# Optimization experiments

Hardware: AMD Instinct MI355X
Metric: run time of the kernel (lower is better)

The kernel has to match this reference:

```python
import jax, jax.numpy as jnp
import numpy as np
from jax import lax

ALPHA = 1.0
NEG = -1.0e6  # sentinel 'no foreground' position; squared dist ~1e12 fits fp32


def _edt(fg):
    """Exact Euclidean distance transform: distance from every pixel to the
    nearest True pixel of fg [B, H, W] (0 where fg is True). Matches
    scipy.ndimage.distance_transform_edt(1 - mask) with mask = fg.
    Separable algorithm: exact 1D pass along W, then exact min over rows."""
    B, H, W = fg.shape
    xi = jnp.arange(W, dtype=jnp.float32)
    # nearest foreground to the LEFT (j <= i): max index j with fg
    pos_l = jnp.where(fg, xi, NEG)
    dl = xi - lax.cummax(pos_l, axis=2)
    # nearest foreground to the RIGHT (j >= i): min index j with fg
    pos_r = jnp.where(fg, -xi, NEG)
    right = lax.cummax(pos_r[..., ::-1], axis=2)[..., ::-1]  # = -min_{j>=i} j
    dr = -right - xi
    g2 = jnp.square(jnp.minimum(dl, dr))  # [B, H, W] squared 1D distance

    y = jnp.arange(H, dtype=jnp.float32)
    sq = jnp.square(y[:, None] - y[None, :])  # [H, H] (y - y')^2

    def col_pass(g2_img):  # [H, W] -> [H, W]
        # dt2[y, x] = min_{y'} g2[y', x] + (y - y')^2  (exact 2D EDT^2)
        return jnp.min(g2_img[None, :, :] + sq[:, :, None], axis=1)

    dt2 = lax.map(col_pass, g2)  # sequential over batch to bound memory
    return jnp.sqrt(dt2)


def setup_inputs() -> dict:
    key = jax.random.key(0)
    k1, k2 = jax.random.split(key)
    pred = jax.random.normal(k1, (16, 2, 256, 256), dtype=jnp.float32)
    target = jax.random.randint(k2, (16, 256, 256), 0, 2, dtype=jnp.int32)
    return {"pred": pred, "target": target}


def reference(pred, target):
    # pred: [B, C, H, W] logits; target: [B, H, W] binary int mask
    pred_lbl = jnp.argmax(pred, axis=1)  # [B, H, W] in {0, 1} (C == 2)
    pred_dt = lax.stop_gradient(_edt(pred_lbl == 1))
    tgt_dt = lax.stop_gradient(_edt(target == 1))
    hd_p2t = jnp.mean(pred_lbl.astype(jnp.float32) * tgt_dt)
    hd_t2p = jnp.mean(target.astype(jnp.float32) * pred_dt)
    return ALPHA * (hd_p2t + hd_t2p) / 2.0
```

## Files before the change

kernel.cpp:

```cpp
#include <hip/hip_runtime.h>
#include <hip/hip_bf16.h>
#include <math.h>


#define B 16
#define H 256
#define W 256
#define IMG (H * W)
#define NPIX (B * IMG)
#define NEGF (-1.0e6f)
#define NINF (-3.0e38f)
#define NBLK 2048

__global__ __launch_bounds__(256) void rowpass_kernel(
    const float* __restrict__ pred, const int* __restrict__ target,
    float* __restrict__ g2, unsigned char* __restrict__ lbl) {
  const int lane = threadIdx.x & 63;
  const int wid = threadIdx.x >> 6;
  const int row = blockIdx.x * 4 + wid;
  const int m = row >> 12;
  const int bh = row & 4095;
  const int b = bh >> 8;
  const int y = bh & 255;
  const int x0 = lane * 4;

  bool fg[4];
  if (m == 0) {
    const float* base = pred + (size_t)b * (2 * IMG) + y * W + x0;
    const float4 c0 = *(const float4*)(base);
    const float4 c1 = *(const float4*)(base + IMG);
    fg[0] = c1.x > c0.x; fg[1] = c1.y > c0.y;
    fg[2] = c1.z > c0.z; fg[3] = c1.w > c0.w;
  } else {
    const int4 tv = *(const int4*)(target + (size_t)b * IMG + y * W + x0);
    fg[0] = tv.x == 1; fg[1] = tv.y == 1; fg[2] = tv.z == 1; fg[3] = tv.w == 1;
  }

  uchar4 lb;
  lb.x = fg[0]; lb.y = fg[1]; lb.z = fg[2]; lb.w = fg[3];
  *(uchar4*)(lbl + (size_t)m * NPIX + (size_t)b * IMG + y * W + x0) = lb;

  const float xf0 = (float)x0;

  float p0 = fg[0] ? xf0 : NEGF;
  float p1 = fmaxf(p0, fg[1] ? xf0 + 1.f : NEGF);
  float p2 = fmaxf(p1, fg[2] ? xf0 + 2.f : NEGF);
  float p3 = fmaxf(p2, fg[3] ? xf0 + 3.f : NEGF);
  float s = p3;
#pragma unroll
  for (int off = 1; off < 64; off <<= 1) {
    float u = __shfl_up(s, (unsigned)off);
    if (lane >= off) s = fmaxf(s, u);
  }
  float e = __shfl_up(s, 1u);
  if (lane == 0) e = NINF;
  const float dl0 = xf0 - fmaxf(e, p0);
  const float dl1 = xf0 + 1.f - fmaxf(e, p1);
  const float dl2 = xf0 + 2.f - fmaxf(e, p2);
  const float dl3 = xf0 + 3.f - fmaxf(e, p3);

  float q3 = fg[3] ? -(xf0 + 3.f) : NEGF;
  float q2 = fmaxf(q3, fg[2] ? -(xf0 + 2.f) : NEGF);
  float q1 = fmaxf(q2, fg[1] ? -(xf0 + 1.f) : NEGF);
  float q0 = fmaxf(q1, fg[0] ? -xf0 : NEGF);
  float t = q0;
#pragma unroll
  for (int off = 1; off < 64; off <<= 1) {
    float u = __shfl_down(t, (unsigned)off);
    if (lane < 64 - off) t = fmaxf(t, u);
  }
  float f = __shfl_down(t, 1u);
  if (lane == 63) f = NINF;
  const float dr0 = -fmaxf(f, q0) - xf0;
  const float dr1 = -fmaxf(f, q1) - (xf0 + 1.f);
  const float dr2 = -fmaxf(f, q2) - (xf0 + 2.f);
  const float dr3 = -fmaxf(f, q3) - (xf0 + 3.f);

  float4 o;
  float v;
  v = fminf(dl0, dr0); o.x = v * v;
  v = fminf(dl1, dr1); o.y = v * v;
  v = fminf(dl2, dr2); o.z = v * v;
  v = fminf(dl3, dr3); o.w = v * v;
  *(float4*)(g2 + (size_t)m * NPIX + (size_t)b * IMG + y * W + x0) = o;
}

__global__ __launch_bounds__(256) void colpass_kernel(
    const float* __restrict__ g2, const unsigned char* __restrict__ lbl,
    float* __restrict__ partials) {
  const int tid = threadIdx.x;
  const int bi = blockIdx.x;
  const int xt = bi & 3;
  const int yt = (bi >> 2) & 15;
  const int m = (bi >> 6) & 1;
  const int b = bi >> 7;
  const int xin = tid & 63;
  const int ysub = tid >> 6;
  const int x = xt * 64 + xin;
  const int y0 = yt * 16 + ysub * 4;

  const float* __restrict__ gimg = g2 + (size_t)m * NPIX + (size_t)b * IMG;

  float a0 = gimg[(y0 + 0) * W + x];
  float a1 = gimg[(y0 + 1) * W + x];
  float a2 = gimg[(y0 + 2) * W + x];
  float a3 = gimg[(y0 + 3) * W + x];

  const float U = fmaxf(fmaxf(a0, a1), fmaxf(a2, a3));
  const int r = (int)sqrtf(U) + 1;
  int lo = y0 - r; if (lo < 0) lo = 0;
  int hi = y0 + 3 + r; if (hi > H - 1) hi = H - 1;

  for (int yp = lo; yp <= hi; ++yp) {
    const float v = gimg[yp * W + x];
    const float d0 = (float)(y0 - yp);
    const float d1 = d0 + 1.f;
    const float d2 = d0 + 2.f;
    const float d3 = d0 + 3.f;
    a0 = fminf(a0, fmaf(d0, d0, v));
    a1 = fminf(a1, fmaf(d1, d1, v));
    a2 = fminf(a2, fmaf(d2, d2, v));
    a3 = fminf(a3, fmaf(d3, d3, v));
  }

  const unsigned char* wl =
      lbl + (size_t)(1 - m) * NPIX + (size_t)b * IMG + y0 * W + x;
  float local = 0.f;
  local += (float)wl[0 * W] * sqrtf(a0);
  local += (float)wl[1 * W] * sqrtf(a1);
  local += (float)wl[2 * W] * sqrtf(a2);
  local += (float)wl[3 * W] * sqrtf(a3);

  __shared__ float red[256];
  red[tid] = local;
  __syncthreads();
  for (int s = 128; s > 0; s >>= 1) {
    if (tid < s) red[tid] += red[tid + s];
    __syncthreads();
  }
  if (tid == 0) partials[bi] = red[0];
}

__global__ __launch_bounds__(256) void finalize_kernel(
    const float* __restrict__ partials, float* __restrict__ out) {
  const int tid = threadIdx.x;
  float s = 0.f;
#pragma unroll
  for (int i = 0; i < NBLK / 256; ++i) s += partials[i * 256 + tid];
  __shared__ float red[256];
  red[tid] = s;
  __syncthreads();
  for (int k = 128; k > 0; k >>= 1) {
    if (tid < k) red[tid] += red[tid + k];
    __syncthreads();
  }
  if (tid == 0) out[0] = red[0] * (0.5f / (float)NPIX);
}

extern "C" void kernel_launch(void* const* d_in, const int* in_sizes, int n_in,
                              void* d_out, int out_size, void* d_ws, size_t ws_size,
                              hipStream_t stream) {
  const float* pred = (const float*)d_in[0];
  const int* target = (const int*)d_in[1];
  float* out = (float*)d_out;

  float* g2 = (float*)d_ws;
  float* partials = g2 + 2 * (size_t)NPIX;
  unsigned char* lbl = (unsigned char*)(partials + NBLK);

  rowpass_kernel<<<2 * B * H / 4, 256, 0, stream>>>(pred, target, g2, lbl);
  colpass_kernel<<<NBLK, 256, 0, stream>>>(g2, lbl, partials);
  finalize_kernel<<<1, 256, 0, stream>>>(partials, out);
}
```

Measured before the change: 77.70 us.

## Fuse row pass, column pass and final reduction into one cooperative kernel

Merges the three launches into a single cooperative-launch kernel of 1024 persistent blocks, with grid-wide syncs between the row pass, the column pass and the final reduction. Each block now handles two row groups and two column tiles. This removes two kernel launch gaps and the separate finalize launch. In exchange it adds two grid barriers, which are costly across all CUs, and fixes the grid size, which must fit co-resident at 4 blocks per CU.

```diff
diff --git a/kernel.cpp b/kernel.cpp
--- a/kernel.cpp
+++ b/kernel.cpp
@@ -1,6 +1,9 @@
 #include <hip/hip_runtime.h>
 #include <hip/hip_bf16.h>
+#include <hip/hip_cooperative_groups.h>
 #include <math.h>
+
+namespace cg = cooperative_groups;
 
 
 #define B 16
@@ -10,151 +13,156 @@
 #define NPIX (B * IMG)
 #define NEGF (-1.0e6f)
 #define NINF (-3.0e38f)
-#define NBLK 2048
+#define GRID 1024
 
-__global__ __launch_bounds__(256) void rowpass_kernel(
+__global__ __launch_bounds__(256, 4) void fused_kernel(
     const float* __restrict__ pred, const int* __restrict__ target,
-    float* __restrict__ g2, unsigned char* __restrict__ lbl) {
-  const int lane = threadIdx.x & 63;
-  const int wid = threadIdx.x >> 6;
-  const int row = blockIdx.x * 4 + wid;
-  const int m = row >> 12;
-  const int bh = row & 4095;
-  const int b = bh >> 8;
-  const int y = bh & 255;
-  const int x0 = lane * 4;
+    float* __restrict__ g2, unsigned char* __restrict__ lbl,
+    float* __restrict__ partials, float* __restrict__ out) {
+  cg::grid_group grid = cg::this_grid();
+  const int tid = threadIdx.x;
+  const int lane = tid & 63;
+  const int wid = tid >> 6;
+  __shared__ float red[256];
 
-  bool fg[4];
-  if (m == 0) {
-    const float* base = pred + (size_t)b * (2 * IMG) + y * W + x0;
-    const float4 c0 = *(const float4*)(base);
-    const float4 c1 = *(const float4*)(base + IMG);
-    fg[0] = c1.x > c0.x; fg[1] = c1.y > c0.y;
-    fg[2] = c1.z > c0.z; fg[3] = c1.w > c0.w;
-  } else {
-    const int4 tv = *(const int4*)(target + (size_t)b * IMG + y * W + x0);
-    fg[0] = tv.x == 1; fg[1] = tv.y == 1; fg[2] = tv.z == 1; fg[3] = tv.w == 1;
+#pragma unroll
+  for (int i = 0; i < 2; ++i) {
+    const int row = blockIdx.x * 8 + i * 4 + wid;
+    const int m = row >> 12;
+    const int bh = row & 4095;
+    const int b = bh >> 8;
+    const int y = bh & 255;
+    const int x0 = lane * 4;
+
+    bool fg[4];
+    if (m == 0) {
+      const float* base = pred + (size_t)b * (2 * IMG) + y * W + x0;
+      const float4 c0 = *(const float4*)(base);
+      const float4 c1 = *(const float4*)(base + IMG);
+      fg[0] = c1.x > c0.x; fg[1] = c1.y > c0.y;
+      fg[2] = c1.z > c0.z; fg[3] = c1.w > c0.w;
+    } else {
+      const int4 tv = *(const int4*)(target + (size_t)b * IMG + y * W + x0);
+      fg[0] = tv.x == 1; fg[1] = tv.y == 1; fg[2] = tv.z == 1; fg[3] = tv.w == 1;
+    }
+
+    uchar4 lb;
+    lb.x = fg[0]; lb.y = fg[1]; lb.z = fg[2]; lb.w = fg[3];
+    *(uchar4*)(lbl + (size_t)m * NPIX + (size_t)b * IMG + y * W + x0) = lb;
+
+    const float xf0 = (float)x0;
+
+    float p0 = fg[0] ? xf0 : NEGF;
+    float p1 = fmaxf(p0, fg[1] ? xf0 + 1.f : NEGF);
+    float p2 = fmaxf(p1, fg[2] ? xf0 + 2.f : NEGF);
+    float p3 = fmaxf(p2, fg[3] ? xf0 + 3.f : NEGF);
+    float s = p3;
+#pragma unroll
+    for (int off = 1; off < 64; off <<= 1) {
+      float u = __shfl_up(s, (unsigned)off);
+      if (lane >= off) s = fmaxf(s, u);
+    }
+    float e = __shfl_up(s, 1u);
+    if (lane == 0) e = NINF;
+    const float dl0 = xf0 - fmaxf(e, p0);
+    const float dl1 = xf0 + 1.f - fmaxf(e, p1);
+    const float dl2 = xf0 + 2.f - fmaxf(e, p2);
+    const float dl3 = xf0 + 3.f - fmaxf(e, p3);
+
+    float q3 = fg[3] ? -(xf0 + 3.f) : NEGF;
+    float q2 = fmaxf(q3, fg[2] ? -(xf0 + 2.f) : NEGF);
+    float q1 = fmaxf(q2, fg[1] ? -(xf0 + 1.f) : NEGF);
+    float q0 = fmaxf(q1, fg[0] ? -xf0 : NEGF);
+    float t = q0;
+#pragma unroll
+    for (int off = 1; off < 64; off <<= 1) {
+      float u = __shfl_down(t, (unsigned)off);
+      if (lane < 64 - off) t = fmaxf(t, u);
+    }
+    float f = __shfl_down(t, 1u);
+    if (lane == 63) f = NINF;
+    const float dr0 = -fmaxf(f, q0) - xf0;
+    const float dr1 = -fmaxf(f, q1) - (xf0 + 1.f);
+    const float dr2 = -fmaxf(f, q2) - (xf0 + 2.f);
+    const float dr3 = -fmaxf(f, q3) - (xf0 + 3.f);
+
+    float4 o;
+    float v;
+    v = fminf(dl0, dr0); o.x = v * v;
+    v = fminf(dl1, dr1); o.y = v * v;
+    v = fminf(dl2, dr2); o.z = v * v;
+    v = fminf(dl3, dr3); o.w = v * v;
+    *(float4*)(g2 + (size_t)m * NPIX + (size_t)b * IMG + y * W + x0) = o;
   }
 
-  uchar4 lb;
-  lb.x = fg[0]; lb.y = fg[1]; lb.z = fg[2]; lb.w = fg[3];
-  *(uchar4*)(lbl + (size_t)m * NPIX + (size_t)b * IMG + y * W + x0) = lb;
+  grid.sync();
 
-  const float xf0 = (float)x0;
+  float local = 0.f;
+#pragma unroll
+  for (int t2 = 0; t2 < 2; ++t2) {
+    const int ti = blockIdx.x + t2 * GRID;
+    const int xt = ti & 3;
+    const int yt = (ti >> 2) & 15;
+    const int m = (ti >> 6) & 1;
+    const int b = ti >> 7;
+    const int xin = tid & 63;
+    const int ysub = tid >> 6;
+    const int x = xt * 64 + xin;
+    const int y0 = yt * 16 + ysub * 4;
 
-  float p0 = fg[0] ? xf0 : NEGF;
-  float p1 = fmaxf(p0, fg[1] ? xf0 + 1.f : NEGF);
-  float p2 = fmaxf(p1, fg[2] ? xf0 + 2.f : NEGF);
-  float p3 = fmaxf(p2, fg[3] ? xf0 + 3.f : NEGF);
-  float s = p3;
-#pragma unroll
-  for (int off = 1; off < 64; off <<= 1) {
-    float u = __shfl_up(s, (unsigned)off);
-    if (lane >= off) s = fmaxf(s, u);
-  }
-  float e = __shfl_up(s, 1u);
-  if (lane == 0) e = NINF;
-  const float dl0 = xf0 - fmaxf(e, p0);
-  const float dl1 = xf0 + 1.f - fmaxf(e, p1);
-  const float dl2 = xf0 + 2.f - fmaxf(e, p2);
-  const float dl3 = xf0 + 3.f - fmaxf(e, p3);
+    const float* __restrict__ gimg = g2 + (size_t)m * NPIX + (size_t)b * IMG;
 
-  float q3 = fg[3] ? -(xf0 + 3.f) : NEGF;
-  float q2 = fmaxf(q3, fg[2] ? -(xf0 + 2.f) : NEGF);
-  float q1 = fmaxf(q2, fg[1] ? -(xf0 + 1.f) : NEGF);
-  float q0 = fmaxf(q1, fg[0] ? -xf0 : NEGF);
-  float t = q0;
-#pragma unroll
-  for (int off = 1; off < 64; off <<= 1) {
-    float u = __shfl_down(t, (unsigned)off);
-    if (lane < 64 - off) t = fmaxf(t, u);
-  }
-  float f = __shfl_down(t, 1u);
-  if (lane == 63) f = NINF;
-  const float dr0 = -fmaxf(f, q0) - xf0;
-  const float dr1 = -fmaxf(f, q1) - (xf0 + 1.f);
-  const float dr2 = -fmaxf(f, q2) - (xf0 + 2.f);
-  const float dr3 = -fmaxf(f, q3) - (xf0 + 3.f);
+    float a0 = gimg[(y0 + 0) * W + x];
+    float a1 = gimg[(y0 + 1) * W + x];
+    float a2 = gimg[(y0 + 2) * W + x];
+    float a3 = gimg[(y0 + 3) * W + x];
 
-  float4 o;
-  float v;
-  v = fminf(dl0, dr0); o.x = v * v;
-  v = fminf(dl1, dr1); o.y = v * v;
-  v = fminf(dl2, dr2); o.z = v * v;
-  v = fminf(dl3, dr3); o.w = v * v;
-  *(float4*)(g2 + (size_t)m * NPIX + (size_t)b * IMG + y * W + x0) = o;
-}
+    const float U = fmaxf(fmaxf(a0, a1), fmaxf(a2, a3));
+    const int r = (int)sqrtf(U) + 1;
+    int lo = y0 - r; if (lo < 0) lo = 0;
+    int hi = y0 + 3 + r; if (hi > H - 1) hi = H - 1;
 
-__global__ __launch_bounds__(256) void colpass_kernel(
-    const float* __restrict__ g2, const unsigned char* __restrict__ lbl,
-    float* __restrict__ partials) {
-  const int tid = threadIdx.x;
-  const int bi = blockIdx.x;
-  const int xt = bi & 3;
-  const int yt = (bi >> 2) & 15;
-  const int m = (bi >> 6) & 1;
-  const int b = bi >> 7;
-  const int xin = tid & 63;
-  const int ysub = tid >> 6;
-  const int x = xt * 64 + xin;
-  const int y0 = yt * 16 + ysub * 4;
+    for (int yp = lo; yp <= hi; ++yp) {
+      const float v = gimg[yp * W + x];
+      const float d0 = (float)(y0 - yp);
+      const float d1 = d0 + 1.f;
+      const float d2 = d0 + 2.f;
+      const float d3 = d0 + 3.f;
+      a0 = fminf(a0, fmaf(d0, d0, v));
+      a1 = fminf(a1, fmaf(d1, d1, v));
+      a2 = fminf(a2, fmaf(d2, d2, v));
+      a3 = fminf(a3, fmaf(d3, d3, v));
+    }
 
-  const float* __restrict__ gimg = g2 + (size_t)m * NPIX + (size_t)b * IMG;
-
-  float a0 = gimg[(y0 + 0) * W + x];
-  float a1 = gimg[(y0 + 1) * W + x];
-  float a2 = gimg[(y0 + 2) * W + x];
-  float a3 = gimg[(y0 + 3) * W + x];
-
-  const float U = fmaxf(fmaxf(a0, a1), fmaxf(a2, a3));
-  const int r = (int)sqrtf(U) + 1;
-  int lo = y0 - r; if (lo < 0) lo = 0;
-  int hi = y0 + 3 + r; if (hi > H - 1) hi = H - 1;
-
-  for (int yp = lo; yp <= hi; ++yp) {
-    const float v = gimg[yp * W + x];
-    const float d0 = (float)(y0 - yp);
-    const float d1 = d0 + 1.f;
-    const float d2 = d0 + 2.f;
-    const float d3 = d0 + 3.f;
-    a0 = fminf(a0, fmaf(d0, d0, v));
-    a1 = fminf(a1, fmaf(d1, d1, v));
-    a2 = fminf(a2, fmaf(d2, d2, v));
-    a3 = fminf(a3, fmaf(d3, d3, v));
+    const unsigned char* wl =
+        lbl + (size_t)(1 - m) * NPIX + (size_t)b * IMG + y0 * W + x;
+    local += (float)wl[0 * W] * sqrtf(a0);
+    local += (float)wl[1 * W] * sqrtf(a1);
+    local += (float)wl[2 * W] * sqrtf(a2);
+    local += (float)wl[3 * W] * sqrtf(a3);
   }
 
-  const unsigned char* wl =
-      lbl + (size_t)(1 - m) * NPIX + (size_t)b * IMG + y0 * W + x;
-  float local = 0.f;
-  local += (float)wl[0 * W] * sqrtf(a0);
-  local += (float)wl[1 * W] * sqrtf(a1);
-  local += (float)wl[2 * W] * sqrtf(a2);
-  local += (float)wl[3 * W] * sqrtf(a3);
-
-  __shared__ float red[256];
   red[tid] = local;
   __syncthreads();
   for (int s = 128; s > 0; s >>= 1) {
     if (tid < s) red[tid] += red[tid + s];
     __syncthreads();
   }
-  if (tid == 0) partials[bi] = red[0];
-}
+  if (tid == 0) partials[blockIdx.x] = red[0];
 
-__global__ __launch_bounds__(256) void finalize_kernel(
-    const float* __restrict__ partials, float* __restrict__ out) {
-  const int tid = threadIdx.x;
-  float s = 0.f;
-#pragma unroll
-  for (int i = 0; i < NBLK / 256; ++i) s += partials[i * 256 + tid];
-  __shared__ float red[256];
-  red[tid] = s;
-  __syncthreads();
-  for (int k = 128; k > 0; k >>= 1) {
-    if (tid < k) red[tid] += red[tid + k];
+  grid.sync();
+
+  if (blockIdx.x == 0) {
+    float s = partials[tid] + partials[tid + 256] +
+              partials[tid + 512] + partials[tid + 768];
+    red[tid] = s;
     __syncthreads();
+    for (int k = 128; k > 0; k >>= 1) {
+      if (tid < k) red[tid] += red[tid + k];
+      __syncthreads();
+    }
+    if (tid == 0) out[0] = red[0] * (0.5f / (float)NPIX);
   }
-  if (tid == 0) out[0] = red[0] * (0.5f / (float)NPIX);
 }
 
 extern "C" void kernel_launch(void* const* d_in, const int* in_sizes, int n_in,
@@ -166,9 +174,10 @@
 
   float* g2 = (float*)d_ws;
   float* partials = g2 + 2 * (size_t)NPIX;
-  unsigned char* lbl = (unsigned char*)(partials + NBLK);
+  unsigned char* lbl = (unsigned char*)(partials + GRID);
 
-  rowpass_kernel<<<2 * B * H / 4, 256, 0, stream>>>(pred, target, g2, lbl);
-  colpass_kernel<<<NBLK, 256, 0, stream>>>(g2, lbl, partials);
-  finalize_kernel<<<1, 256, 0, stream>>>(partials, out);
+  void* args[] = {(void*)&pred, (void*)&target, (void*)&g2,
+                  (void*)&lbl, (void*)&partials, (void*)&out};
+  hipLaunchCooperativeKernel((void*)fused_kernel, dim3(GRID), dim3(256),
+                             args, 0, stream);
 }
```

After: 275.8 us. 3.55x slower.
